# Optimization experiments

Measured on AMD Instinct MI355X. Metric: run time of the kernel, lower is better.

The kernel has to match this reference:

```python
import jax, jax.numpy as jnp
import numpy as np

DIM = 1024
NHEADS = 16
DIM_HEAD = 64
HIDDEN = NHEADS * DIM_HEAD  # 1024


def _xavier(key, fan_in, fan_out):
    limit = np.sqrt(6.0 / (fan_in + fan_out))
    return jax.random.uniform(key, (fan_in, fan_out), jnp.float32, -limit, limit)


def setup_inputs() -> dict:
    key = jax.random.key(0)
    kq, k1, k2, k3 = jax.random.split(key, 4)
    q = jax.random.normal(kq, (2, 2048, DIM), jnp.float32)
    Wq = _xavier(k1, DIM, HIDDEN)
    bq = jnp.zeros((HIDDEN,), jnp.float32)
    Wkv = _xavier(k2, DIM, 2 * HIDDEN)
    bkv = jnp.zeros((2 * HIDDEN,), jnp.float32)
    Wo = _xavier(k3, HIDDEN, DIM)
    bo = jnp.zeros((DIM,), jnp.float32)
    return {"q": q, "Wq": Wq, "bq": bq, "Wkv": Wkv, "bkv": bkv, "Wo": Wo, "bo": bo}


def reference(q, Wq, bq, Wkv, bkv, Wo, bo):
    scale = DIM_HEAD ** (-0.5)
    query = q @ Wq + bq                      # [b, s, hidden]
    kv = q @ Wkv + bkv                       # self-attention: kv from q
    key_, value = jnp.split(kv, 2, axis=-1)  # [b, s, hidden] each
    b, s, _ = query.shape
    query = query.reshape(b, s, NHEADS, DIM_HEAD)
    key_ = key_.reshape(b, s, NHEADS, DIM_HEAD)
    value = value.reshape(b, s, NHEADS, DIM_HEAD)
    scores = jnp.einsum('bqhd,bkhd->bhqk', query, key_) * scale
    attn = jax.nn.softmax(scores, axis=-1)
    out = jnp.einsum('bhqk,bkhd->bqhd', attn, value)
    out = out.reshape(b, s, HIDDEN)
    return out @ Wo + bo
```

## Files before the change

kernel.cpp:

```cpp
#include <hip/hip_runtime.h>

#define DIM 1024
#define NHEADS 16
#define DH 64
#define BATCH 2
#define SEQ 2048

typedef float f32x4 __attribute__((ext_vector_type(4)));
typedef short s16x8 __attribute__((ext_vector_type(8)));
typedef short s16x4 __attribute__((ext_vector_type(4)));

__device__ __forceinline__ short f2bf(float f) {
    union { float f; unsigned u; } v; v.f = f;
    unsigned r = v.u + 0x7fffu + ((v.u >> 16) & 1u);
    return (short)(r >> 16);
}

__device__ __forceinline__ void gld16(const void* g, void* l) {
    __builtin_amdgcn_global_load_lds(
        (const __attribute__((address_space(1))) void*)g,
        (__attribute__((address_space(3))) void*)l, 16, 0, 0);
}

__global__ __launch_bounds__(256) void convert_bf16_kernel(
    const float* __restrict__ X, short* __restrict__ Y)
{
    const int i = (blockIdx.x * 256 + threadIdx.x) * 8;
    float4 a = *(const float4*)(X + i);
    float4 b = *(const float4*)(X + i + 4);
    s16x8 o;
    o[0] = f2bf(a.x); o[1] = f2bf(a.y); o[2] = f2bf(a.z); o[3] = f2bf(a.w);
    o[4] = f2bf(b.x); o[5] = f2bf(b.y); o[6] = f2bf(b.z); o[7] = f2bf(b.w);
    *(s16x8*)(Y + i) = o;
}

__global__ __launch_bounds__(256) void transpose_bf16_kernel(
    const float* __restrict__ W, short* __restrict__ WT, int N)
{
    const int t  = threadIdx.x;
    const int n  = blockIdx.x * 64 + (t & 63);
    const int k0 = (blockIdx.y * 4 + (t >> 6)) * 8;
    s16x8 o;
#pragma unroll
    for (int j = 0; j < 8; ++j) o[j] = f2bf(W[(size_t)(k0 + j) * N + n]);
    *(s16x8*)&WT[(size_t)n * 1024 + k0] = o;
}

template<int TM, bool OUT_BF16>
__global__ __launch_bounds__(256) void gemm_mfma_kernel(
    const short* __restrict__ A, const short* __restrict__ Bt,
    const float* __restrict__ bias0, const float* __restrict__ bias1, int nsplit,
    void* __restrict__ C, int M, int N)
{
    const int K = 1024;
    constexpr int NI = (TM == 128) ? 4 : 2;
    __shared__ short As[TM * 32];
    __shared__ short Bs[128 * 32];

    const int t    = threadIdx.x;
    const int wave = t >> 6;
    const int lane = t & 63;
    const int col  = lane & 15;
    const int quad = lane >> 4;
    const int m0 = blockIdx.y * TM;
    const int n0 = blockIdx.x * 128;
    const int wroff = (TM == 128) ? (wave >> 1) * 64 : 0;
    const int wcoff = (TM == 128) ? (wave & 1) * 64 : wave * 32;

    f32x4 acc[4][NI];
#pragma unroll
    for (int mi = 0; mi < 4; ++mi)
#pragma unroll
        for (int ni = 0; ni < NI; ++ni) acc[mi][ni] = (f32x4){0.f, 0.f, 0.f, 0.f};

    constexpr int RPW = TM / 4;
    const int ldrowA = wave * RPW + (lane >> 2);
    const int ldrowB = wave * 32  + (lane >> 2);
    const int ldcol  = (lane & 3) * 8;
    const short* Ag = A  + (size_t)(m0 + ldrowA) * K + ldcol;
    const short* Bg = Bt + (size_t)(n0 + ldrowB) * K + ldcol;
    short* AsW = &As[wave * RPW * 32];
    short* BsW = &Bs[wave * 1024];

    for (int k0 = 0; k0 < K; k0 += 32) {
        __syncthreads();
        gld16(Ag + k0, AsW);
        if (TM == 128) gld16(Ag + 16 * K + k0, AsW + 512);
        gld16(Bg + k0,          BsW);
        gld16(Bg + 16 * K + k0, BsW + 512);
        __syncthreads();

        s16x8 aA[4], bB[NI];
#pragma unroll
        for (int mi = 0; mi < 4; ++mi)
            aA[mi] = *(const s16x8*)&As[(wroff + 16 * mi + col) * 32 + quad * 8];
#pragma unroll
        for (int ni = 0; ni < NI; ++ni)
            bB[ni] = *(const s16x8*)&Bs[(wcoff + 16 * ni + col) * 32 + quad * 8];
#pragma unroll
        for (int mi = 0; mi < 4; ++mi)
#pragma unroll
            for (int ni = 0; ni < NI; ++ni)
                acc[mi][ni] = __builtin_amdgcn_mfma_f32_16x16x32_bf16(aA[mi], bB[ni], acc[mi][ni], 0, 0, 0);
    }

    float bias_v[NI];
#pragma unroll
    for (int ni = 0; ni < NI; ++ni) {
        int nb = n0 + wcoff + 16 * ni + col;
        bias_v[ni] = (nb < nsplit) ? bias0[nb] : bias1[nb - nsplit];
    }

#pragma unroll
    for (int mi = 0; mi < 4; ++mi)
#pragma unroll
        for (int ni = 0; ni < NI; ++ni)
#pragma unroll
            for (int r = 0; r < 4; ++r) {
                const int gm = m0 + wroff + 16 * mi + quad * 4 + r;
                const int gn = n0 + wcoff + 16 * ni + col;
                float v = acc[mi][ni][r] + bias_v[ni];
                if (OUT_BF16) ((short*)C)[(size_t)gm * N + gn] = f2bf(v);
                else          ((float*)C)[(size_t)gm * N + gn] = v;
            }
}

__global__ __launch_bounds__(512) void attn_v5_kernel(
    const short* __restrict__ QKV,
    short* __restrict__ O)
{
    const int qt = blockIdx.x;
    const int h  = blockIdx.y;
    const int b  = blockIdx.z;
    const int t  = threadIdx.x;
    const int wave = t >> 6;
    const int lane = t & 63;
    const int col  = lane & 15;
    const int quad = lane >> 4;
    const int wq = wave & 3;
    const int kh = wave >> 2;

    __shared__ short Ks[2][64 * 72];
    __shared__ short Vt[2][64 * 72];
    __shared__ short Ps[8][64 * 40];

    const short* Qg = QKV + (size_t)(b * SEQ + qt * 256) * 3072 + h * DH;
    const short* Kg = QKV + (size_t)(b * SEQ) * 3072 + 1024 + h * DH;
    const short* Vg = Kg + 1024;

    s16x8 aQ[4][2];
#pragma unroll
    for (int tq = 0; tq < 4; ++tq)
#pragma unroll
        for (int kq = 0; kq < 2; ++kq)
            aQ[tq][kq] = *(const s16x8*)(Qg + (size_t)(wq * 64 + 16 * tq + col) * 3072 + kq * 32 + quad * 8);

    f32x4 oa[4][4];
    float lsum[4] = {0.f, 0.f, 0.f, 0.f};
#pragma unroll
    for (int td = 0; td < 4; ++td)
#pragma unroll
        for (int tq = 0; tq < 4; ++tq) oa[td][tq] = (f32x4){0.f, 0.f, 0.f, 0.f};

    const int srow = t >> 3;
    const int sc8  = (t & 7) * 8;
    const short* KgS = Kg + (size_t)srow * 3072 + sc8;
    const short* VgS = Vg + (size_t)srow * 3072 + sc8;
    s16x8 kx = *(const s16x8*)KgS;
    s16x8 vx = *(const s16x8*)VgS;

    short* PsW = &Ps[wave][0];

    for (int kt = 0; kt < SEQ / 64; ++kt) {
        const int cur = kt & 1;
        *(s16x8*)&Ks[cur][srow * 72 + sc8] = kx;
#pragma unroll
        for (int jj = 0; jj < 8; ++jj) {
            int dv = sc8 + jj;
            Vt[cur][dv * 72 + (srow & 7) + 8 * (((srow >> 3) ^ (dv >> 3)) & 7)] = vx[jj];
        }
        {
            int nt = (kt + 1 < SEQ / 64) ? kt + 1 : kt;
            kx = *(const s16x8*)(KgS + (size_t)nt * 64 * 3072);
            vx = *(const s16x8*)(VgS + (size_t)nt * 64 * 3072);
        }
        __syncthreads();

        s16x8 aK[2][2];
#pragma unroll
        for (int tk = 0; tk < 2; ++tk)
#pragma unroll
            for (int kq = 0; kq < 2; ++kq)
                aK[tk][kq] = *(const s16x8*)&Ks[cur][(kh * 32 + 16 * tk + col) * 72 + kq * 32 + quad * 8];
        f32x4 st[2][4];
#pragma unroll
        for (int tk = 0; tk < 2; ++tk)
#pragma unroll
            for (int tq = 0; tq < 4; ++tq) {
                f32x4 a = (f32x4){0.f, 0.f, 0.f, 0.f};
                a = __builtin_amdgcn_mfma_f32_16x16x32_bf16(aK[tk][0], aQ[tq][0], a, 0, 0, 0);
                a = __builtin_amdgcn_mfma_f32_16x16x32_bf16(aK[tk][1], aQ[tq][1], a, 0, 0, 0);
                st[tk][tq] = a;
            }

#pragma unroll
        for (int tk = 0; tk < 2; ++tk)
#pragma unroll
            for (int tq = 0; tq < 4; ++tq) {
                float p0 = __expf(st[tk][tq][0] * 0.125f);
                float p1 = __expf(st[tk][tq][1] * 0.125f);
                float p2 = __expf(st[tk][tq][2] * 0.125f);
                float p3 = __expf(st[tk][tq][3] * 0.125f);
                lsum[tq] += (p0 + p1) + (p2 + p3);
                s16x4 pk;
                pk[0] = f2bf(p0); pk[1] = f2bf(p1); pk[2] = f2bf(p2); pk[3] = f2bf(p3);
                *(s16x4*)&PsW[(16 * tq + col) * 40 + 16 * tk + quad * 4] = pk;
            }
        asm volatile("s_waitcnt lgkmcnt(0)" ::: "memory");

        s16x8 bP[4];
#pragma unroll
        for (int tq = 0; tq < 4; ++tq)
            bP[tq] = *(const s16x8*)&PsW[(16 * tq + col) * 40 + quad * 8];
#pragma unroll
        for (int td = 0; td < 4; ++td) {
            const int dv = 16 * td + col;
            s16x8 aV = *(const s16x8*)&Vt[cur][dv * 72 + 8 * (((kh * 4 + quad) ^ (dv >> 3)) & 7)];
#pragma unroll
            for (int tq = 0; tq < 4; ++tq)
                oa[td][tq] = __builtin_amdgcn_mfma_f32_16x16x32_bf16(aV, bP[tq], oa[td][tq], 0, 0, 0);
        }
    }

#pragma unroll
    for (int tq = 0; tq < 4; ++tq) {
        lsum[tq] += __shfl_xor(lsum[tq], 16);
        lsum[tq] += __shfl_xor(lsum[tq], 32);
    }

    __syncthreads();
    float* red  = (float*)&Ps[0][0];
    float* redl = red + 8192;
#pragma unroll
    for (int round = 0; round < 2; ++round) {
        if (wave >= 4 && ((wave >> 1) & 1) == round) {
            const int slot = wave & 1;
#pragma unroll
            for (int td = 0; td < 4; ++td)
#pragma unroll
                for (int tq = 0; tq < 4; ++tq)
#pragma unroll
                    for (int r = 0; r < 4; ++r)
                        red[slot * 4096 + (16 * td + quad * 4 + r) * 64 + 16 * tq + col] = oa[td][tq][r];
            if (quad == 0)
#pragma unroll
                for (int tq = 0; tq < 4; ++tq)
                    redl[slot * 64 + 16 * tq + col] = lsum[tq];
        }
        __syncthreads();
        if (wave < 4 && ((wave >> 1) & 1) == round) {
            const int slot = wave & 1;
#pragma unroll
            for (int td = 0; td < 4; ++td)
#pragma unroll
                for (int tq = 0; tq < 4; ++tq)
#pragma unroll
                    for (int r = 0; r < 4; ++r)
                        oa[td][tq][r] += red[slot * 4096 + (16 * td + quad * 4 + r) * 64 + 16 * tq + col];
#pragma unroll
            for (int tq = 0; tq < 4; ++tq)
                lsum[tq] += redl[slot * 64 + 16 * tq + col];
        }
        __syncthreads();
    }

    if (wave < 4) {
        short* Og = O + (size_t)(b * SEQ + qt * 256 + wq * 64) * DIM + h * DH;
        float inv[4];
#pragma unroll
        for (int tq = 0; tq < 4; ++tq) inv[tq] = 1.f / lsum[tq];
#pragma unroll
        for (int td = 0; td < 4; ++td)
#pragma unroll
            for (int tq = 0; tq < 4; ++tq) {
                s16x4 v;
#pragma unroll
                for (int r = 0; r < 4; ++r) v[r] = f2bf(oa[td][tq][r] * inv[tq]);
                *(s16x4*)(Og + (size_t)(16 * tq + col) * DIM + 16 * td + quad * 4) = v;
            }
    }
}

extern "C" void kernel_launch(void* const* d_in, const int* in_sizes, int n_in,
                              void* d_out, int out_size, void* d_ws, size_t ws_size,
                              hipStream_t stream)
{
    const float* q   = (const float*)d_in[0];
    const float* Wq  = (const float*)d_in[1];
    const float* bq  = (const float*)d_in[2];
    const float* Wkv = (const float*)d_in[3];
    const float* bkv = (const float*)d_in[4];
    const float* Wo  = (const float*)d_in[5];
    const float* bo  = (const float*)d_in[6];
    float* out = (float*)d_out;

    const int M = BATCH * SEQ;

    short* qb     = (short*)d_ws;
    short* WqkvT  = qb     + (size_t)M * DIM;
    short* WoT    = WqkvT  + (size_t)3 * DIM * DIM;
    short* QKVbuf = WoT    + (size_t)DIM * DIM;
    short* AObuf  = QKVbuf + (size_t)M * 3 * DIM;

    convert_bf16_kernel<<<(M * DIM) / (256 * 8), 256, 0, stream>>>(q, qb);
    transpose_bf16_kernel<<<dim3(DIM / 64, 32), 256, 0, stream>>>(Wq, WqkvT, DIM);
    transpose_bf16_kernel<<<dim3(2 * DIM / 64, 32), 256, 0, stream>>>(Wkv, WqkvT + (size_t)DIM * DIM, 2 * DIM);
    transpose_bf16_kernel<<<dim3(DIM / 64, 32), 256, 0, stream>>>(Wo, WoT, DIM);

    gemm_mfma_kernel<128, true><<<dim3(3 * DIM / 128, M / 128), 256, 0, stream>>>(
        qb, WqkvT, bq, bkv, DIM, QKVbuf, M, 3 * DIM);
    attn_v5_kernel<<<dim3(SEQ / 256, NHEADS, BATCH), 512, 0, stream>>>(QKVbuf, AObuf);
    gemm_mfma_kernel<64, false><<<dim3(DIM / 128, M / 64), 256, 0, stream>>>(
        AObuf, WoT, bo, bo, 1 << 30, out, M, DIM);
}
```

Measured before the change: 202.6 us.

## Pre-transpose V globally, fold softmax scale into Q, fuse weight transposes, packed bf16 cvt

```diff
diff --git a/kernel.cpp b/kernel.cpp
--- a/kernel.cpp
+++ b/kernel.cpp
@@ -16,6 +16,35 @@
     return (short)(r >> 16);
 }
 
+#if defined(__has_builtin)
+#if __has_builtin(__builtin_amdgcn_cvt_pk_bf16_f32)
+#define HAVE_PK_BF16 1
+#endif
+#endif
+__device__ __forceinline__ unsigned f2bf_pk(float a, float b) {
+#ifdef HAVE_PK_BF16
+    typedef __bf16 bf16x2_t __attribute__((ext_vector_type(2)));
+    bf16x2_t r = __builtin_amdgcn_cvt_pk_bf16_f32(a, b);
+    return __builtin_bit_cast(unsigned, r);
+#else
+    return ((unsigned)(unsigned short)f2bf(b) << 16) | (unsigned short)f2bf(a);
+#endif
+}
+__device__ __forceinline__ s16x4 pk4(float a, float b, float c, float d) {
+    union { unsigned u[2]; s16x4 v; } x;
+    x.u[0] = f2bf_pk(a, b); x.u[1] = f2bf_pk(c, d);
+    return x.v;
+}
+
+#if defined(__has_builtin)
+#if __has_builtin(__builtin_amdgcn_exp2f)
+#define EXP2(x) __builtin_amdgcn_exp2f(x)
+#endif
+#endif
+#ifndef EXP2
+#define EXP2(x) exp2f(x)
+#endif
+
 __device__ __forceinline__ void gld16(const void* g, void* l) {
     __builtin_amdgcn_global_load_lds(
         (const __attribute__((address_space(1))) void*)g,
@@ -28,29 +57,63 @@
     const int i = (blockIdx.x * 256 + threadIdx.x) * 8;
     float4 a = *(const float4*)(X + i);
     float4 b = *(const float4*)(X + i + 4);
-    s16x8 o;
-    o[0] = f2bf(a.x); o[1] = f2bf(a.y); o[2] = f2bf(a.z); o[3] = f2bf(a.w);
-    o[4] = f2bf(b.x); o[5] = f2bf(b.y); o[6] = f2bf(b.z); o[7] = f2bf(b.w);
-    *(s16x8*)(Y + i) = o;
-}
-
-__global__ __launch_bounds__(256) void transpose_bf16_kernel(
-    const float* __restrict__ W, short* __restrict__ WT, int N)
+    union { unsigned u[4]; s16x8 v; } o;
+    o.u[0] = f2bf_pk(a.x, a.y); o.u[1] = f2bf_pk(a.z, a.w);
+    o.u[2] = f2bf_pk(b.x, b.y); o.u[3] = f2bf_pk(b.z, b.w);
+    *(s16x8*)(Y + i) = o.v;
+}
+
+__global__ __launch_bounds__(256) void transpose_w_kernel(
+    const float* __restrict__ Wq, const float* __restrict__ Wkv,
+    const float* __restrict__ Wo, short* __restrict__ WT)
 {
     const int t  = threadIdx.x;
-    const int n  = blockIdx.x * 64 + (t & 63);
+    const int ng = blockIdx.x * 64 + (t & 63);
     const int k0 = (blockIdx.y * 4 + (t >> 6)) * 8;
-    s16x8 o;
-#pragma unroll
-    for (int j = 0; j < 8; ++j) o[j] = f2bf(W[(size_t)(k0 + j) * N + n]);
-    *(s16x8*)&WT[(size_t)n * 1024 + k0] = o;
+    const float* W; int n, N;
+    if (ng < 1024)      { W = Wq;  n = ng;        N = 1024; }
+    else if (ng < 3072) { W = Wkv; n = ng - 1024; N = 2048; }
+    else                { W = Wo;  n = ng - 3072; N = 1024; }
+    float v[8];
+#pragma unroll
+    for (int j = 0; j < 8; ++j) v[j] = W[(size_t)(k0 + j) * N + n];
+    union { unsigned u[4]; s16x8 s; } o;
+    o.u[0] = f2bf_pk(v[0], v[1]); o.u[1] = f2bf_pk(v[2], v[3]);
+    o.u[2] = f2bf_pk(v[4], v[5]); o.u[3] = f2bf_pk(v[6], v[7]);
+    *(s16x8*)&WT[(size_t)ng * 1024 + k0] = o.s;
+}
+
+__global__ __launch_bounds__(256) void transpose_v_kernel(
+    const short* __restrict__ QKV, short* __restrict__ VtG)
+{
+    const int t = threadIdx.x;
+    const int tok0 = blockIdx.x * 64;
+    const int h = blockIdx.y, b = blockIdx.z;
+    __shared__ short L[64 * 72];
+    const short* src = QKV + (size_t)(b * SEQ + tok0) * 3072 + 2048 + h * 64;
+#pragma unroll
+    for (int p = 0; p < 2; ++p) {
+        int r = p * 32 + (t >> 3);
+        *(s16x8*)&L[r * 72 + (t & 7) * 8] = *(const s16x8*)(src + (size_t)r * 3072 + (t & 7) * 8);
+    }
+    __syncthreads();
+    short* dst = VtG + (size_t)(b * NHEADS + h) * 64 * SEQ + tok0;
+#pragma unroll
+    for (int p = 0; p < 2; ++p) {
+        int u = p * 256 + t;
+        int dv = u >> 3, c = (u & 7) * 8;
+        s16x8 o;
+#pragma unroll
+        for (int j = 0; j < 8; ++j) o[j] = L[(c + j) * 72 + dv];
+        *(s16x8*)(dst + (size_t)dv * SEQ + c) = o;
+    }
 }
 
 template<int TM, bool OUT_BF16>
 __global__ __launch_bounds__(256) void gemm_mfma_kernel(
     const short* __restrict__ A, const short* __restrict__ Bt,
     const float* __restrict__ bias0, const float* __restrict__ bias1, int nsplit,
-    void* __restrict__ C, int M, int N)
+    float s0, float s1, void* __restrict__ C, int M, int N)
 {
     const int K = 1024;
     constexpr int NI = (TM == 128) ? 4 : 2;
@@ -104,11 +167,12 @@
                 acc[mi][ni] = __builtin_amdgcn_mfma_f32_16x16x32_bf16(aA[mi], bB[ni], acc[mi][ni], 0, 0, 0);
     }
 
-    float bias_v[NI];
+    float bias_v[NI], scale_v[NI];
 #pragma unroll
     for (int ni = 0; ni < NI; ++ni) {
         int nb = n0 + wcoff + 16 * ni + col;
-        bias_v[ni] = (nb < nsplit) ? bias0[nb] : bias1[nb - nsplit];
+        bias_v[ni]  = (nb < nsplit) ? bias0[nb] : bias1[nb - nsplit];
+        scale_v[ni] = (nb < nsplit) ? s0 : s1;
     }
 
 #pragma unroll
@@ -119,14 +183,15 @@
             for (int r = 0; r < 4; ++r) {
                 const int gm = m0 + wroff + 16 * mi + quad * 4 + r;
                 const int gn = n0 + wcoff + 16 * ni + col;
-                float v = acc[mi][ni][r] + bias_v[ni];
+                float v = (acc[mi][ni][r] + bias_v[ni]) * scale_v[ni];
                 if (OUT_BF16) ((short*)C)[(size_t)gm * N + gn] = f2bf(v);
                 else          ((float*)C)[(size_t)gm * N + gn] = v;
             }
 }
 
-__global__ __launch_bounds__(512) void attn_v5_kernel(
+__global__ __launch_bounds__(512) void attn_v6_kernel(
     const short* __restrict__ QKV,
+    const short* __restrict__ VtG,
     short* __restrict__ O)
 {
     const int qt = blockIdx.x;
@@ -146,7 +211,7 @@
 
     const short* Qg = QKV + (size_t)(b * SEQ + qt * 256) * 3072 + h * DH;
     const short* Kg = QKV + (size_t)(b * SEQ) * 3072 + 1024 + h * DH;
-    const short* Vg = Kg + 1024;
+    const short* VtRow = VtG + (size_t)(b * NHEADS + h) * 64 * SEQ;
 
     s16x8 aQ[4][2];
 #pragma unroll
@@ -164,25 +229,21 @@
 
     const int srow = t >> 3;
     const int sc8  = (t & 7) * 8;
-    const short* KgS = Kg + (size_t)srow * 3072 + sc8;
-    const short* VgS = Vg + (size_t)srow * 3072 + sc8;
+    const short* KgS  = Kg + (size_t)srow * 3072 + sc8;
+    const short* VtgS = VtRow + (size_t)srow * SEQ + sc8;
     s16x8 kx = *(const s16x8*)KgS;
-    s16x8 vx = *(const s16x8*)VgS;
+    s16x8 vx = *(const s16x8*)VtgS;
 
     short* PsW = &Ps[wave][0];
 
     for (int kt = 0; kt < SEQ / 64; ++kt) {
         const int cur = kt & 1;
         *(s16x8*)&Ks[cur][srow * 72 + sc8] = kx;
-#pragma unroll
-        for (int jj = 0; jj < 8; ++jj) {
-            int dv = sc8 + jj;
-            Vt[cur][dv * 72 + (srow & 7) + 8 * (((srow >> 3) ^ (dv >> 3)) & 7)] = vx[jj];
-        }
+        *(s16x8*)&Vt[cur][srow * 72 + sc8] = vx;
         {
             int nt = (kt + 1 < SEQ / 64) ? kt + 1 : kt;
             kx = *(const s16x8*)(KgS + (size_t)nt * 64 * 3072);
-            vx = *(const s16x8*)(VgS + (size_t)nt * 64 * 3072);
+            vx = *(const s16x8*)(VtgS + (size_t)nt * 64);
         }
         __syncthreads();
 
@@ -207,14 +268,12 @@
         for (int tk = 0; tk < 2; ++tk)
 #pragma unroll
             for (int tq = 0; tq < 4; ++tq) {
-                float p0 = __expf(st[tk][tq][0] * 0.125f);
-                float p1 = __expf(st[tk][tq][1] * 0.125f);
-                float p2 = __expf(st[tk][tq][2] * 0.125f);
-                float p3 = __expf(st[tk][tq][3] * 0.125f);
+                float p0 = EXP2(st[tk][tq][0]);
+                float p1 = EXP2(st[tk][tq][1]);
+                float p2 = EXP2(st[tk][tq][2]);
+                float p3 = EXP2(st[tk][tq][3]);
                 lsum[tq] += (p0 + p1) + (p2 + p3);
-                s16x4 pk;
-                pk[0] = f2bf(p0); pk[1] = f2bf(p1); pk[2] = f2bf(p2); pk[3] = f2bf(p3);
-                *(s16x4*)&PsW[(16 * tq + col) * 40 + 16 * tk + quad * 4] = pk;
+                *(s16x4*)&PsW[(16 * tq + col) * 40 + 16 * tk + quad * 4] = pk4(p0, p1, p2, p3);
             }
         asm volatile("s_waitcnt lgkmcnt(0)" ::: "memory");
 
@@ -225,7 +284,7 @@
 #pragma unroll
         for (int td = 0; td < 4; ++td) {
             const int dv = 16 * td + col;
-            s16x8 aV = *(const s16x8*)&Vt[cur][dv * 72 + 8 * (((kh * 4 + quad) ^ (dv >> 3)) & 7)];
+            s16x8 aV = *(const s16x8*)&Vt[cur][dv * 72 + kh * 32 + quad * 8];
 #pragma unroll
             for (int tq = 0; tq < 4; ++tq)
                 oa[td][tq] = __builtin_amdgcn_mfma_f32_16x16x32_bf16(aV, bP[tq], oa[td][tq], 0, 0, 0);
@@ -282,12 +341,10 @@
 #pragma unroll
         for (int td = 0; td < 4; ++td)
 #pragma unroll
-            for (int tq = 0; tq < 4; ++tq) {
-                s16x4 v;
-#pragma unroll
-                for (int r = 0; r < 4; ++r) v[r] = f2bf(oa[td][tq][r] * inv[tq]);
-                *(s16x4*)(Og + (size_t)(16 * tq + col) * DIM + 16 * td + quad * 4) = v;
-            }
+            for (int tq = 0; tq < 4; ++tq)
+                *(s16x4*)(Og + (size_t)(16 * tq + col) * DIM + 16 * td + quad * 4) =
+                    pk4(oa[td][tq][0] * inv[tq], oa[td][tq][1] * inv[tq],
+                        oa[td][tq][2] * inv[tq], oa[td][tq][3] * inv[tq]);
     }
 }
 
@@ -307,19 +364,20 @@
     const int M = BATCH * SEQ;
 
     short* qb     = (short*)d_ws;
-    short* WqkvT  = qb     + (size_t)M * DIM;
-    short* WoT    = WqkvT  + (size_t)3 * DIM * DIM;
-    short* QKVbuf = WoT    + (size_t)DIM * DIM;
+    short* WT     = qb     + (size_t)M * DIM;
+    short* QKVbuf = WT     + (size_t)4096 * DIM;
     short* AObuf  = QKVbuf + (size_t)M * 3 * DIM;
+    short* VtG    = (short*)d_out;
+
+    const float QSCALE = 0.18033688011112042f;
 
     convert_bf16_kernel<<<(M * DIM) / (256 * 8), 256, 0, stream>>>(q, qb);
-    transpose_bf16_kernel<<<dim3(DIM / 64, 32), 256, 0, stream>>>(Wq, WqkvT, DIM);
-    transpose_bf16_kernel<<<dim3(2 * DIM / 64, 32), 256, 0, stream>>>(Wkv, WqkvT + (size_t)DIM * DIM, 2 * DIM);
-    transpose_bf16_kernel<<<dim3(DIM / 64, 32), 256, 0, stream>>>(Wo, WoT, DIM);
+    transpose_w_kernel<<<dim3(64, 32), 256, 0, stream>>>(Wq, Wkv, Wo, WT);
 
     gemm_mfma_kernel<128, true><<<dim3(3 * DIM / 128, M / 128), 256, 0, stream>>>(
-        qb, WqkvT, bq, bkv, DIM, QKVbuf, M, 3 * DIM);
-    attn_v5_kernel<<<dim3(SEQ / 256, NHEADS, BATCH), 512, 0, stream>>>(QKVbuf, AObuf);
+        qb, WT, bq, bkv, DIM, QSCALE, 1.0f, QKVbuf, M, 3 * DIM);
+    transpose_v_kernel<<<dim3(SEQ / 64, NHEADS, BATCH), 256, 0, stream>>>(QKVbuf, VtG);
+    attn_v6_kernel<<<dim3(SEQ / 256, NHEADS, BATCH), 512, 0, stream>>>(QKVbuf, VtG, AObuf);
     gemm_mfma_kernel<64, false><<<dim3(DIM / 128, M / 64), 256, 0, stream>>>(
-        AObuf, WoT, bo, bo, 1 << 30, out, M, DIM);
-}
+        AObuf, WT + (size_t)3072 * 1024, bo, bo, 1 << 30, 1.0f, 1.0f, out, M, DIM);
+}
```

Result: no change. 199.7 us (-1.4%).
